# Performance work log

Hardware: AMD Instinct MI355X
Metric: run time of the kernel (lower is better)

Reference implementation:

```python
import jax, jax.numpy as jnp
import numpy as np

N = 50000      # num nodes
E = 600000     # num edges
D = 128        # num_node_features (in == out)
R = 8          # num_relations


def setup_inputs() -> dict:
    key = jax.random.key(0)
    k = jax.random.split(key, 6)
    x = jax.random.normal(k[0], (N, D), dtype=jnp.float32)
    edge_index = jax.random.randint(k[1], (2, E), 0, N, dtype=jnp.int32)
    edge_type = jax.random.randint(k[2], (E,), 0, R, dtype=jnp.int32)
    scale = 1.0 / np.sqrt(D).astype(np.float32)
    weight = jax.random.normal(k[3], (R, D, D), dtype=jnp.float32) * scale  # per-relation W_r
    root = jax.random.normal(k[4], (D, D), dtype=jnp.float32) * scale       # self-loop weight
    bias = jnp.zeros((D,), dtype=jnp.float32)
    return {"x": x, "edge_index": edge_index, "edge_type": edge_type,
            "weight": weight, "root": root, "bias": bias}


def _rgcn(x, weight, root, bias, edge_index, edge_type):
    # RGCNConv (PyG defaults: aggr='mean' per relation, root weight + bias)
    src, dst = edge_index[0], edge_index[1]
    # combined segment id over (relation, dst) so one segment_sum covers all relations
    seg = edge_type * N + dst                              # [E]
    msgs = x[src]                                          # [E, D] gather
    sums = jax.ops.segment_sum(msgs, seg, num_segments=R * N)                 # [R*N, D]
    cnts = jax.ops.segment_sum(jnp.ones((E, 1), x.dtype), seg, num_segments=R * N)
    mean = sums / jnp.maximum(cnts, 1.0)                   # mean over neighbors, 0 if none
    agg = mean.reshape(R, N, D)
    out = jnp.einsum('rnd,rde->ne', agg, weight) + x @ root + bias
    return out


def reference(x, edge_index, edge_type, weight, root, bias):
    return jax.nn.relu(_rgcn(x, weight, root, bias, edge_index, edge_type))
```

## Files before the change

kernel.cpp:

```cpp
#include <hip/hip_runtime.h>

constexpr int NN = 50000;
constexpr int NE = 600000;
constexpr int D  = 128;
constexpr int NR = 8;
constexpr int KT = (NR + 1) * D;
constexpr int NSEG = NN * NR;

constexpr int SCAN_ELEMS = 1024;
constexpr int NBLK2 = (NSEG + SCAN_ELEMS - 1) / SCAN_ELEMS;

typedef unsigned int   u32;
typedef unsigned short u16;
typedef float  f32x4 __attribute__((ext_vector_type(4)));
typedef short  s16x8 __attribute__((ext_vector_type(8)));

__device__ __forceinline__ u16 f2bf(float f) {
    u32 u = __float_as_uint(f);
    u32 r = (u + 0x7fffu + ((u >> 16) & 1u)) >> 16;
    return (u16)r;
}

__device__ __forceinline__ void async_cp16(const void* g, void* l) {
    __builtin_amdgcn_global_load_lds(
        (const __attribute__((address_space(1))) u32*)g,
        (__attribute__((address_space(3))) u32*)l, 16, 0, 0);
}

__global__ __launch_bounds__(256) void prep_all(const float* __restrict__ x,
                                                const float* __restrict__ weight,
                                                const float* __restrict__ root,
                                                const int* __restrict__ dst,
                                                const int* __restrict__ et,
                                                u16* __restrict__ xb,
                                                u16* __restrict__ wt9,
                                                int* __restrict__ cnt2) {
    const int NX4 = NN * D / 4;
    const int NW  = (NR + 1) * D * D;
    int gid = blockIdx.x * 256 + threadIdx.x;
    if (gid < NX4) {
        int i = gid * 4;
        float4 v = *(const float4*)(x + i);
        ushort4 o;
        o.x = f2bf(v.x); o.y = f2bf(v.y); o.z = f2bf(v.z); o.w = f2bf(v.w);
        *(ushort4*)(xb + i) = o;
        return;
    }
    int g = gid - NX4;
    if (g < NW) {
        int p = g >> 14;
        int idx = g & 16383;
        int n = idx >> 7, k = idx & 127;
        float v = (p == 0) ? root[k * D + n]
                           : weight[(size_t)(p - 1) * D * D + k * D + n];
        wt9[(size_t)p * 16384 + idx] = f2bf(v);
        return;
    }
    int e = g - NW;
    if (e < NE) atomicAdd(&cnt2[dst[e] * NR + et[e]], 1);
}

__global__ __launch_bounds__(256) void scan1(const int* __restrict__ cnt,
                                             int* __restrict__ offs,
                                             int* __restrict__ bsums) {
    __shared__ int lds[256];
    int t = threadIdx.x;
    int base = blockIdx.x * SCAN_ELEMS + t * 4;
    int v0 = (base + 0 < NSEG) ? cnt[base + 0] : 0;
    int v1 = (base + 1 < NSEG) ? cnt[base + 1] : 0;
    int v2 = (base + 2 < NSEG) ? cnt[base + 2] : 0;
    int v3 = (base + 3 < NSEG) ? cnt[base + 3] : 0;
    int s = v0 + v1 + v2 + v3;
    lds[t] = s;
    __syncthreads();
    int val = s;
    for (int off = 1; off < 256; off <<= 1) {
        int tmp = (t >= off) ? lds[t - off] : 0;
        __syncthreads();
        val += tmp;
        lds[t] = val;
        __syncthreads();
    }
    int ex = val - s;
    if (base + 0 < NSEG) offs[base + 0] = ex;
    if (base + 1 < NSEG) offs[base + 1] = ex + v0;
    if (base + 2 < NSEG) offs[base + 2] = ex + v0 + v1;
    if (base + 3 < NSEG) offs[base + 3] = ex + v0 + v1 + v2;
    if (t == 255) bsums[blockIdx.x] = val;
}

__global__ __launch_bounds__(512) void scan2(int* __restrict__ bsums) {
    __shared__ int lds[512];
    int t = threadIdx.x;
    int v = (t < NBLK2) ? bsums[t] : 0;
    lds[t] = v;
    __syncthreads();
    int val = v;
    for (int off = 1; off < 512; off <<= 1) {
        int tmp = (t >= off) ? lds[t - off] : 0;
        __syncthreads();
        val += tmp;
        lds[t] = val;
        __syncthreads();
    }
    if (t < NBLK2) bsums[t] = val - v;
}

__global__ __launch_bounds__(256) void scan3(int* __restrict__ offs,
                                             int* __restrict__ cur,
                                             const int* __restrict__ bsums) {
    int i = blockIdx.x * 256 + threadIdx.x;
    if (i < NSEG) {
        int v = offs[i] + bsums[i >> 10];
        offs[i] = v;
        cur[i]  = v;
    }
    if (i == 0) offs[NSEG] = NE;
}

__global__ __launch_bounds__(256) void fill_bins(const int* __restrict__ src,
                                                 const int* __restrict__ dst,
                                                 const int* __restrict__ et,
                                                 int* __restrict__ cur,
                                                 int* __restrict__ ebin) {
    int e = blockIdx.x * 256 + threadIdx.x;
    if (e >= NE) return;
    int r = et[e];
    int idx = atomicAdd(&cur[dst[e] * NR + r], 1);
    ebin[idx] = (r << 16) | src[e];
}

__global__ __launch_bounds__(128) void aggregate_kernel(const u32* __restrict__ xw,
                                                        const int* __restrict__ offs2,
                                                        const int* __restrict__ ebin,
                                                        u32* __restrict__ sw) {
    const int lane = threadIdx.x & 63;
    const int n = blockIdx.x * 2 + (threadIdx.x >> 6);
    if (n >= NN) return;
    const int beg = __builtin_amdgcn_readfirstlane(offs2[n * NR]);
    const int c   = __builtin_amdgcn_readfirstlane(offs2[n * NR + NR]) - beg;

    float a0 = 0.f, a1 = 0.f;
    int r_cur = 0, cnt_cur = 0;

    int q0 = 0, q1 = 0, q2 = 0, q3 = 0, q4 = 0, q5 = 0, q6 = 0, q7 = 0;
    u32 v0 = 0, v1 = 0, v2 = 0, v3 = 0, v4 = 0, v5 = 0, v6 = 0, v7 = 0;

#define REFILL(Q, V, IDX)                                                   \
    if ((IDX) < c) {                                                        \
        Q = __builtin_amdgcn_readfirstlane(ebin[beg + (IDX)]);              \
        V = xw[(size_t)((u32)Q & 0xffffu) * 64 + lane];                     \
    }
#define FLUSH()                                                             \
    {                                                                       \
        float inv_ = 1.0f / (float)(cnt_cur > 0 ? cnt_cur : 1);             \
        u32 lo16_ = f2bf(a0 * inv_);                                        \
        u32 hi16_ = f2bf(a1 * inv_);                                        \
        sw[((size_t)r_cur * NN + n) * 64 + lane] = lo16_ | (hi16_ << 16);   \
        a0 = 0.f; a1 = 0.f; cnt_cur = 0; ++r_cur;                           \
    }
#define CONSUME(Q, V)                                                       \
    {                                                                       \
        int rj_ = (int)((u32)(Q) >> 16);                                    \
        while (r_cur < rj_) FLUSH()                                         \
        a0 += __uint_as_float((V) << 16);                                   \
        a1 += __uint_as_float((V) & 0xffff0000u);                           \
        ++cnt_cur;                                                          \
    }

    REFILL(q0, v0, 0) REFILL(q1, v1, 1) REFILL(q2, v2, 2) REFILL(q3, v3, 3)
    REFILL(q4, v4, 4) REFILL(q5, v5, 5) REFILL(q6, v6, 6) REFILL(q7, v7, 7)

    int e = 0;
    for (; e + 8 <= c; e += 8) {
        CONSUME(q0, v0) REFILL(q0, v0, e + 8)
        CONSUME(q1, v1) REFILL(q1, v1, e + 9)
        CONSUME(q2, v2) REFILL(q2, v2, e + 10)
        CONSUME(q3, v3) REFILL(q3, v3, e + 11)
        CONSUME(q4, v4) REFILL(q4, v4, e + 12)
        CONSUME(q5, v5) REFILL(q5, v5, e + 13)
        CONSUME(q6, v6) REFILL(q6, v6, e + 14)
        CONSUME(q7, v7) REFILL(q7, v7, e + 15)
    }
    if (e + 0 < c) CONSUME(q0, v0)
    if (e + 1 < c) CONSUME(q1, v1)
    if (e + 2 < c) CONSUME(q2, v2)
    if (e + 3 < c) CONSUME(q3, v3)
    if (e + 4 < c) CONSUME(q4, v4)
    if (e + 5 < c) CONSUME(q5, v5)
    if (e + 6 < c) CONSUME(q6, v6)
    if (e + 7 < c) CONSUME(q7, v7)

    while (r_cur < NR) FLUSH()
#undef REFILL
#undef FLUSH
#undef CONSUME
}

__global__ __launch_bounds__(256) void mfma_gemm(const u16* __restrict__ xb,
                                                 const u16* __restrict__ sums,
                                                 const u16* __restrict__ wt9,
                                                 const float* __restrict__ bias,
                                                 float* __restrict__ out) {
    __shared__ __align__(16) u16 Bs[4][2][128 * 32];

    const int tid  = threadIdx.x;
    const int wave = tid >> 6;
    const int lane = tid & 63;
    const int m0   = blockIdx.x * 128;
    const int fr   = lane & 15;
    const int fk   = (lane >> 4) * 8;

    int boff[8];
#pragma unroll
    for (int r = 0; r < 8; ++r) {
        int p = r * 64 + lane;
        int g = p ^ ((p >> 3) & 7);
        boff[r] = (g >> 2) * D + (g & 3) * 8;
    }
    int bidx[8];
#pragma unroll
    for (int nt = 0; nt < 8; ++nt) {
        int gl = (nt * 16 + fr) * 4 + (lane >> 4);
        int pp = gl ^ ((gl >> 3) & 7);
        bidx[nt] = pp * 8;
    }

    int r0 = m0 + wave * 32 + fr;        if (r0 > NN - 1) r0 = NN - 1;
    int r1 = m0 + wave * 32 + 16 + fr;   if (r1 > NN - 1) r1 = NN - 1;
    const size_t aoff0 = (size_t)r0 * D + fk;
    const size_t aoff1 = (size_t)r1 * D + fk;

    u16* myB0 = &Bs[wave][0][0];
    u16* myB1 = &Bs[wave][1][0];

    auto stage = [&](u16* bufp, const u16* Bp) {
#pragma unroll
        for (int r = 0; r < 8; ++r)
            async_cp16(Bp + boff[r], (char*)bufp + (r * 64 + lane) * 16);
    };

    f32x4 acc[2][8];
#pragma unroll
    for (int i = 0; i < 2; ++i)
#pragma unroll
        for (int j = 0; j < 8; ++j) acc[i][j] = (f32x4){0.f, 0.f, 0.f, 0.f};

    stage(myB0, wt9);
    __builtin_amdgcn_sched_barrier(0);
    s16x8 a0c = *(const s16x8*)(xb + aoff0);
    s16x8 a1c = *(const s16x8*)(xb + aoff1);

    for (int it = 0; it < KT / 32 - 1; ++it) {
        const int nx  = it + 1;
        const int rpl = nx >> 2;
        const int kof = (nx & 3) * 32;
        u16* nbuf = (nx & 1) ? myB1 : myB0;
        const u16* cbuf = (it & 1) ? myB1 : myB0;

        stage(nbuf, wt9 + rpl * (D * D) + kof);
        __builtin_amdgcn_sched_barrier(0);
        const u16* Ap = ((rpl == 0) ? xb : sums + (size_t)(rpl - 1) * NN * D) + kof;
        s16x8 a0n = *(const s16x8*)(Ap + aoff0);
        s16x8 a1n = *(const s16x8*)(Ap + aoff1);
        __builtin_amdgcn_sched_barrier(0);
        asm volatile("s_waitcnt vmcnt(10)" ::: "memory");
#pragma unroll
        for (int nt = 0; nt < 8; ++nt) {
            s16x8 bf = *(const s16x8*)(cbuf + bidx[nt]);
            acc[0][nt] = __builtin_amdgcn_mfma_f32_16x16x32_bf16(a0c, bf, acc[0][nt], 0, 0, 0);
            acc[1][nt] = __builtin_amdgcn_mfma_f32_16x16x32_bf16(a1c, bf, acc[1][nt], 0, 0, 0);
        }
        a0c = a0n; a1c = a1n;
    }
    asm volatile("s_waitcnt vmcnt(0)" ::: "memory");
#pragma unroll
    for (int nt = 0; nt < 8; ++nt) {
        s16x8 bf = *(const s16x8*)(myB1 + bidx[nt]);
        acc[0][nt] = __builtin_amdgcn_mfma_f32_16x16x32_bf16(a0c, bf, acc[0][nt], 0, 0, 0);
        acc[1][nt] = __builtin_amdgcn_mfma_f32_16x16x32_bf16(a1c, bf, acc[1][nt], 0, 0, 0);
    }

    const int cl = lane & 15;
    const int rq = (lane >> 4) * 4;
#pragma unroll
    for (int nt = 0; nt < 8; ++nt) {
        int col = nt * 16 + cl;
        float bv = bias[col];
#pragma unroll
        for (int rg = 0; rg < 2; ++rg)
#pragma unroll
            for (int reg = 0; reg < 4; ++reg) {
                int n = m0 + wave * 32 + rg * 16 + rq + reg;
                if (n < NN) {
                    float v = acc[rg][nt][reg] + bv;
                    out[(size_t)n * D + col] = fmaxf(v, 0.0f);
                }
            }
    }
}

extern "C" void kernel_launch(void* const* d_in, const int* in_sizes, int n_in,
                              void* d_out, int out_size, void* d_ws, size_t ws_size,
                              hipStream_t stream) {
    const float* x      = (const float*)d_in[0];
    const int*   ei     = (const int*)d_in[1];
    const int*   et     = (const int*)d_in[2];
    const float* weight = (const float*)d_in[3];
    const float* root   = (const float*)d_in[4];
    const float* bias   = (const float*)d_in[5];
    float* out = (float*)d_out;
    const int* srcv = ei;
    const int* dstv = ei + NE;

    int* cnt2  = (int*)d_ws;
    int* cur2  = cnt2 + NSEG;
    int* offs2 = cur2 + NSEG;
    int* bsums = offs2 + NSEG + 1;
    int* ebin  = bsums + 512;
    size_t fixed_b  = ((char*)(ebin + NE) - (char*)d_ws);
    size_t fixed_al = (fixed_b + 255) & ~(size_t)255;
    u16* xb   = (u16*)((char*)d_ws + fixed_al);
    u16* sums = xb + (size_t)NN * D;
    u16* wt9  = sums + (size_t)NR * NN * D;

    hipMemsetAsync(cnt2, 0, NSEG * sizeof(int), stream);

    const int PREP = NN * D / 4 + (NR + 1) * D * D + NE;
    prep_all<<<(PREP + 255) / 256, 256, 0, stream>>>(x, weight, root, dstv, et,
                                                     xb, wt9, cnt2);

    scan1<<<NBLK2, 256, 0, stream>>>(cnt2, offs2, bsums);
    scan2<<<1, 512, 0, stream>>>(bsums);
    scan3<<<(NSEG + 256) / 256, 256, 0, stream>>>(offs2, cur2, bsums);
    fill_bins<<<(NE + 255) / 256, 256, 0, stream>>>(srcv, dstv, et, cur2, ebin);

    aggregate_kernel<<<(NN + 1) / 2, 128, 0, stream>>>((const u32*)xb, offs2, ebin,
                                                       (u32*)sums);

    mfma_gemm<<<(NN + 127) / 128, 256, 0, stream>>>(xb, sums, wt9, bias, out);
}
```

Baseline: 237.2 us.

## Share weight tiles across waves in GEMM with 64-row blocks and K=64 steps

The final GEMM used to give each wave its own private double-buffered copy of the weight K-slices. It now stages one shared 128x64 weight tile per block, cooperatively loaded by all 256 threads and guarded by block barriers. Each wave computes 16 rows instead of 32, the K step grows from 32 to 64, and the grid doubles in block count. The goal is to cut redundant global-to-LDS weight traffic and raise occupancy. In exchange it adds two block-wide barriers per iteration and halves the MFMA work per wave between syncs.

New measurement: 219.3 us. 1.08x faster.

```diff
diff --git a/kernel.cpp b/kernel.cpp
--- a/kernel.cpp
+++ b/kernel.cpp
@@ -202,101 +202,113 @@
                                                  const u16* __restrict__ wt9,
                                                  const float* __restrict__ bias,
                                                  float* __restrict__ out) {
-    __shared__ __align__(16) u16 Bs[4][2][128 * 32];
+    __shared__ __align__(16) u16 Bs[2][128 * 64];
 
     const int tid  = threadIdx.x;
     const int wave = tid >> 6;
     const int lane = tid & 63;
-    const int m0   = blockIdx.x * 128;
+    const int m0   = blockIdx.x * 64;
     const int fr   = lane & 15;
-    const int fk   = (lane >> 4) * 8;
-
-    int boff[8];
-#pragma unroll
-    for (int r = 0; r < 8; ++r) {
-        int p = r * 64 + lane;
+    const int l4   = lane >> 4;
+    const int fk   = l4 * 8;
+
+    int boff[4];
+#pragma unroll
+    for (int r = 0; r < 4; ++r) {
+        int p = r * 256 + tid;
         int g = p ^ ((p >> 3) & 7);
-        boff[r] = (g >> 2) * D + (g & 3) * 8;
-    }
-    int bidx[8];
-#pragma unroll
-    for (int nt = 0; nt < 8; ++nt) {
-        int gl = (nt * 16 + fr) * 4 + (lane >> 4);
-        int pp = gl ^ ((gl >> 3) & 7);
-        bidx[nt] = pp * 8;
-    }
-
-    int r0 = m0 + wave * 32 + fr;        if (r0 > NN - 1) r0 = NN - 1;
-    int r1 = m0 + wave * 32 + 16 + fr;   if (r1 > NN - 1) r1 = NN - 1;
-    const size_t aoff0 = (size_t)r0 * D + fk;
-    const size_t aoff1 = (size_t)r1 * D + fk;
-
-    u16* myB0 = &Bs[wave][0][0];
-    u16* myB1 = &Bs[wave][1][0];
+        boff[r] = (g >> 3) * D + (g & 7) * 8;
+    }
+    int bidx[16];
+#pragma unroll
+    for (int h = 0; h < 2; ++h)
+#pragma unroll
+        for (int nt = 0; nt < 8; ++nt) {
+            int gl = (nt * 16 + fr) * 8 + h * 4 + l4;
+            int pp = gl ^ ((gl >> 3) & 7);
+            bidx[h * 8 + nt] = pp * 8;
+        }
+
+    int r0 = m0 + wave * 16 + fr;  if (r0 > NN - 1) r0 = NN - 1;
+    const size_t aoff = (size_t)r0 * D + fk;
 
     auto stage = [&](u16* bufp, const u16* Bp) {
 #pragma unroll
-        for (int r = 0; r < 8; ++r)
-            async_cp16(Bp + boff[r], (char*)bufp + (r * 64 + lane) * 16);
+        for (int r = 0; r < 4; ++r)
+            async_cp16(Bp + boff[r], (char*)bufp + (size_t)(r * 256 + tid) * 16);
     };
 
-    f32x4 acc[2][8];
-#pragma unroll
-    for (int i = 0; i < 2; ++i)
-#pragma unroll
-        for (int j = 0; j < 8; ++j) acc[i][j] = (f32x4){0.f, 0.f, 0.f, 0.f};
-
-    stage(myB0, wt9);
+    f32x4 acc[8];
+#pragma unroll
+    for (int j = 0; j < 8; ++j) acc[j] = (f32x4){0.f, 0.f, 0.f, 0.f};
+
+    stage(&Bs[0][0], wt9);
+    s16x8 a0c = *(const s16x8*)(xb + aoff);
+    s16x8 a1c = *(const s16x8*)(xb + aoff + 32);
     __builtin_amdgcn_sched_barrier(0);
-    s16x8 a0c = *(const s16x8*)(xb + aoff0);
-    s16x8 a1c = *(const s16x8*)(xb + aoff1);
-
-    for (int it = 0; it < KT / 32 - 1; ++it) {
+
+    for (int it = 0; it < 17; ++it) {
         const int nx  = it + 1;
-        const int rpl = nx >> 2;
-        const int kof = (nx & 3) * 32;
-        u16* nbuf = (nx & 1) ? myB1 : myB0;
-        const u16* cbuf = (it & 1) ? myB1 : myB0;
-
-        stage(nbuf, wt9 + rpl * (D * D) + kof);
+        const int npl = nx >> 1;
+        const int kof = (nx & 1) * 64;
+        u16* nbuf = &Bs[nx & 1][0];
+        const u16* cbuf = &Bs[it & 1][0];
+
+        stage(nbuf, wt9 + npl * 16384 + kof);
+        const u16* Ap = ((npl == 0) ? xb : sums + (size_t)(npl - 1) * NN * D) + kof;
+        s16x8 a0n = *(const s16x8*)(Ap + aoff);
+        s16x8 a1n = *(const s16x8*)(Ap + aoff + 32);
         __builtin_amdgcn_sched_barrier(0);
-        const u16* Ap = ((rpl == 0) ? xb : sums + (size_t)(rpl - 1) * NN * D) + kof;
-        s16x8 a0n = *(const s16x8*)(Ap + aoff0);
-        s16x8 a1n = *(const s16x8*)(Ap + aoff1);
+        asm volatile("s_waitcnt vmcnt(6)" ::: "memory");
+        __builtin_amdgcn_s_barrier();
         __builtin_amdgcn_sched_barrier(0);
-        asm volatile("s_waitcnt vmcnt(10)" ::: "memory");
 #pragma unroll
         for (int nt = 0; nt < 8; ++nt) {
             s16x8 bf = *(const s16x8*)(cbuf + bidx[nt]);
-            acc[0][nt] = __builtin_amdgcn_mfma_f32_16x16x32_bf16(a0c, bf, acc[0][nt], 0, 0, 0);
-            acc[1][nt] = __builtin_amdgcn_mfma_f32_16x16x32_bf16(a1c, bf, acc[1][nt], 0, 0, 0);
-        }
+            acc[nt] = __builtin_amdgcn_mfma_f32_16x16x32_bf16(a0c, bf, acc[nt], 0, 0, 0);
+        }
+#pragma unroll
+        for (int nt = 0; nt < 8; ++nt) {
+            s16x8 bf = *(const s16x8*)(cbuf + bidx[8 + nt]);
+            acc[nt] = __builtin_amdgcn_mfma_f32_16x16x32_bf16(a1c, bf, acc[nt], 0, 0, 0);
+        }
+        asm volatile("s_waitcnt lgkmcnt(0)" ::: "memory");
+        __builtin_amdgcn_sched_barrier(0);
+        __builtin_amdgcn_s_barrier();
+        __builtin_amdgcn_sched_barrier(0);
         a0c = a0n; a1c = a1n;
     }
     asm volatile("s_waitcnt vmcnt(0)" ::: "memory");
-#pragma unroll
-    for (int nt = 0; nt < 8; ++nt) {
-        s16x8 bf = *(const s16x8*)(myB1 + bidx[nt]);
-        acc[0][nt] = __builtin_amdgcn_mfma_f32_16x16x32_bf16(a0c, bf, acc[0][nt], 0, 0, 0);
-        acc[1][nt] = __builtin_amdgcn_mfma_f32_16x16x32_bf16(a1c, bf, acc[1][nt], 0, 0, 0);
+    __builtin_amdgcn_s_barrier();
+    __builtin_amdgcn_sched_barrier(0);
+    {
+        const u16* cbuf = &Bs[1][0];
+#pragma unroll
+        for (int nt = 0; nt < 8; ++nt) {
+            s16x8 bf = *(const s16x8*)(cbuf + bidx[nt]);
+            acc[nt] = __builtin_amdgcn_mfma_f32_16x16x32_bf16(a0c, bf, acc[nt], 0, 0, 0);
+        }
+#pragma unroll
+        for (int nt = 0; nt < 8; ++nt) {
+            s16x8 bf = *(const s16x8*)(cbuf + bidx[8 + nt]);
+            acc[nt] = __builtin_amdgcn_mfma_f32_16x16x32_bf16(a1c, bf, acc[nt], 0, 0, 0);
+        }
     }
 
     const int cl = lane & 15;
-    const int rq = (lane >> 4) * 4;
+    const int rq = l4 * 4;
 #pragma unroll
     for (int nt = 0; nt < 8; ++nt) {
         int col = nt * 16 + cl;
         float bv = bias[col];
 #pragma unroll
-        for (int rg = 0; rg < 2; ++rg)
-#pragma unroll
-            for (int reg = 0; reg < 4; ++reg) {
-                int n = m0 + wave * 32 + rg * 16 + rq + reg;
-                if (n < NN) {
-                    float v = acc[rg][nt][reg] + bv;
-                    out[(size_t)n * D + col] = fmaxf(v, 0.0f);
-                }
+        for (int reg = 0; reg < 4; ++reg) {
+            int n = m0 + wave * 16 + rq + reg;
+            if (n < NN) {
+                float v = acc[nt][reg] + bv;
+                out[(size_t)n * D + col] = fmaxf(v, 0.0f);
             }
+        }
     }
 }
 
@@ -338,5 +350,5 @@
     aggregate_kernel<<<(NN + 1) / 2, 128, 0, stream>>>((const u32*)xb, offs2, ebin,
                                                        (u32*)sums);
 
-    mfma_gemm<<<(NN + 127) / 128, 256, 0, stream>>>(xb, sums, wt9, bias, out);
-}
+    mfma_gemm<<<(NN + 63) / 64, 256, 0, stream>>>(xb, sums, wt9, bias, out);
+}
```
